# Kernel optimization log

Hardware: AMD Instinct MI355X
Metric: run time of the kernel (lower is better)

The kernel has to match this reference:

```python
import jax, jax.numpy as jnp
import numpy as np

D_MODEL = 512
NUM_HEADS = 8
NUM_LAYERS = 4
SEQ_LEN = 2048
BATCH = 2
LN_EPS = 1e-5


def _layer_norm(x, g, b):
    mu = jnp.mean(x, axis=-1, keepdims=True)
    var = jnp.mean(jnp.square(x - mu), axis=-1, keepdims=True)
    return (x - mu) * jax.lax.rsqrt(var + LN_EPS) * g + b


def setup_inputs() -> dict:
    key = jax.random.key(0)
    ks = jax.random.split(key, 12)
    d, nl = D_MODEL, NUM_LAYERS
    s = 0.02
    return {
        "x": jax.random.normal(ks[0], (BATCH, SEQ_LEN, d), dtype=jnp.float32),
        "mask": jnp.zeros((1, 1, SEQ_LEN, SEQ_LEN), dtype=jnp.float32),
        "Wqkv": jax.random.normal(ks[1], (nl, d, 3 * d), dtype=jnp.float32) * s,
        "Wout": jax.random.normal(ks[2], (nl, d, d), dtype=jnp.float32) * s,
        "ln_g": jnp.ones((nl, d), dtype=jnp.float32),
        "ln_b": jnp.zeros((nl, d), dtype=jnp.float32),
        "W1": jax.random.normal(ks[3], (nl, d, 4 * d), dtype=jnp.float32) * s,
        "b1": jnp.zeros((nl, 4 * d), dtype=jnp.float32),
        "alpha": jnp.full((nl,), 0.01, dtype=jnp.float32),  # PReLU(init=0.01), scalar per block
        "W2": jax.random.normal(ks[4], (nl, 4 * d, d), dtype=jnp.float32) * s,
        "b2": jnp.zeros((nl, d), dtype=jnp.float32),
        "lnf_g": jnp.ones((d,), dtype=jnp.float32),
        "lnf_b": jnp.zeros((d,), dtype=jnp.float32),
    }


def _encoder(x, mask, Wqkv, Wout, ln_g, ln_b, W1, b1, alpha, W2, b2, lnf_g, lnf_b):
    B, L, d = x.shape
    H = NUM_HEADS
    dh = d // H
    scale = 1.0 / (d ** 0.5)  # NOTE: scales by sqrt(d_model), not head dim (as in source)

    def block(x, p):
        wqkv, wout, g, b, w1, b1_, a, w2, b2_ = p
        qkv = x @ wqkv  # [B, L, 3d]
        q, k, v = jnp.split(qkv, 3, axis=-1)
        # b l (h j) -> b h l j
        to_heads = lambda t: t.reshape(B, L, H, dh).transpose(0, 2, 1, 3)
        q, k, v = to_heads(q) * scale, to_heads(k), to_heads(v)
        e = jnp.einsum('bhlj,bhkj->bhlk', q, k) + mask  # [B, H, L, L]
        att = jnp.nan_to_num(jax.nn.softmax(e, axis=-1))
        # Faithful to source: repeated index takes the DIAGONAL of att,
        # then multiplies elementwise into v (NOT a matmul).
        out = jnp.einsum('bhll,bhlj->bhlj', att, v)
        out = out.transpose(0, 2, 1, 3).reshape(B, L, d)  # b h l j -> b l (h j)
        out = out @ wout
        out_att = _layer_norm(out + x, g, b)
        h = out_att @ w1 + b1_
        h = jnp.where(h >= 0, h, a * h)  # PReLU (dropout=0 in eval)
        h = h @ w2 + b2_
        # same LayerNorm params reused (same nn.LayerNorm instance in source)
        return _layer_norm(h + out_att, g, b), None

    params = (Wqkv, Wout, ln_g, ln_b, W1, b1, alpha, W2, b2)
    x, _ = jax.lax.scan(block, x, params)
    return _layer_norm(x, lnf_g, lnf_b)


def reference(x, mask, Wqkv, Wout, ln_g, ln_b, W1, b1, alpha, W2, b2, lnf_g, lnf_b):
    return _encoder(x, mask, Wqkv, Wout, ln_g, ln_b, W1, b1, alpha, W2, b2, lnf_g, lnf_b)
```

## Files before the change

### kernel.cpp

```cpp
#include <hip/hip_runtime.h>
#include <math.h>

typedef unsigned short u16;
typedef __attribute__((ext_vector_type(8))) short short8;
typedef __attribute__((ext_vector_type(4))) float f32x4;

#define SEQ 2048
#define NHEADS 8
#define NLAYERS 4
#define NROWS 4096
#define SCALE_QK 0.044194173824159216f
#define SCALE_QK_LOG2E 0.06376571201f
#define PART_STRIDE ((size_t)NROWS * 512)

#define GLOAD_LDS(gp, lp) __builtin_amdgcn_global_load_lds( \
    (const __attribute__((address_space(1))) uint4*)(gp), \
    (__attribute__((address_space(3))) uint4*)(lp), 16, 0, 0)

__device__ __forceinline__ float b2f(u16 u){
    union { unsigned int i; float f; } c; c.i = ((unsigned int)u) << 16; return c.f;
}
__device__ __forceinline__ u16 f2b(float f){
    union { float f; unsigned int i; } c; c.f = f;
    unsigned int x = c.i;
    unsigned int r = x + 0x7fffu + ((x >> 16) & 1u);
    return (u16)(r >> 16);
}
__device__ __forceinline__ void unpack8(uint4 u, float* f){
    f[0]=b2f(u.x & 0xffffu); f[1]=b2f(u.x >> 16);
    f[2]=b2f(u.y & 0xffffu); f[3]=b2f(u.y >> 16);
    f[4]=b2f(u.z & 0xffffu); f[5]=b2f(u.z >> 16);
    f[6]=b2f(u.w & 0xffffu); f[7]=b2f(u.w >> 16);
}
__device__ __forceinline__ uint4 pack8(const float* f){
    uint4 u;
    u.x = (unsigned)f2b(f[0]) | ((unsigned)f2b(f[1]) << 16);
    u.y = (unsigned)f2b(f[2]) | ((unsigned)f2b(f[3]) << 16);
    u.z = (unsigned)f2b(f[4]) | ((unsigned)f2b(f[5]) << 16);
    u.w = (unsigned)f2b(f[6]) | ((unsigned)f2b(f[7]) << 16);
    return u;
}

__global__ __launch_bounds__(256)
void cvt_f32_bf16(const float* __restrict__ in, u16* __restrict__ out, int n8){
    int i = blockIdx.x * 256 + threadIdx.x;
    if (i >= n8) return;
    const float4* p = (const float4*)(in + (size_t)i * 8);
    float4 a = p[0], b = p[1];
    float f[8] = {a.x, a.y, a.z, a.w, b.x, b.y, b.z, b.w};
    *((uint4*)(out + (size_t)i * 8)) = pack8(f);
}

__global__ __launch_bounds__(256)
void transpose_layer(const float* __restrict__ wqkv, const float* __restrict__ wout,
                     const float* __restrict__ w1,  const float* __restrict__ w2,
                     u16* __restrict__ qkvT, u16* __restrict__ woutT,
                     u16* __restrict__ w1T,  u16* __restrict__ w2T)
{
    __shared__ float tile[32][33];
    int tid = blockIdx.x;
    const float* src; u16* dst; int R, C, local;
    if (tid < 768)       { src = wqkv; dst = qkvT; R = 512;  C = 1536; local = tid; }
    else if (tid < 1024) { src = wout; dst = woutT; R = 512; C = 512;  local = tid - 768; }
    else if (tid < 2048) { src = w1;   dst = w1T;  R = 512;  C = 2048; local = tid - 1024; }
    else                 { src = w2;   dst = w2T;  R = 2048; C = 512;  local = tid - 2048; }
    int ctiles = C >> 5;
    int c0 = (local % ctiles) * 32, r0 = (local / ctiles) * 32;
    int tx = threadIdx.x & 31, ty = threadIdx.x >> 5;
#pragma unroll
    for (int i = 0; i < 4; i++){
        int r = r0 + ty + i * 8;
        tile[ty + i * 8][tx] = src[(size_t)r * C + c0 + tx];
    }
    __syncthreads();
#pragma unroll
    for (int i = 0; i < 4; i++){
        int c = c0 + ty + i * 8;
        dst[(size_t)c * R + r0 + tx] = f2b(tile[tx][ty + i * 8]);
    }
}

template<int BM, int BN, int SPLITS, bool BF16OUT>
__global__ __launch_bounds__(256)
void gemm3(const u16* __restrict__ A, const u16* __restrict__ Bt,
           float* __restrict__ Cf, u16* __restrict__ Cb,
           const float* __restrict__ bias, const float* __restrict__ alphap,
           int M, int N, int K)
{
    constexpr int WAVES_M = BM / 64;
    constexpr int WAVES_N = 4 / WAVES_M;
    constexpr int WN = BN / WAVES_N;
    constexpr int MT = 4, NT = WN / 16;
    __shared__ __align__(16) u16 As[BM * 64];
    __shared__ __align__(16) u16 Bs[BN * 64];

    const int t = threadIdx.x;
    const int wave = t >> 6, lane = t & 63;
    const int quad = lane >> 4, l16 = lane & 15;
    const int wm = (WAVES_M == 2) ? (wave >> 1) : 0;
    const int wn = (WAVES_M == 2) ? (wave & 1) : wave;
    const int n0 = blockIdx.x * BN;
    const int m0 = blockIdx.y * BM;
    const int lr = lane >> 3;
    const int lc = (lane & 7) << 3;
    const int Ks = K / SPLITS;
    const int kbeg = blockIdx.z * Ks;

    f32x4 acc[MT][NT];
#pragma unroll
    for (int i = 0; i < MT; i++)
#pragma unroll
        for (int j = 0; j < NT; j++) acc[i][j] = (f32x4){0.f, 0.f, 0.f, 0.f};

    for (int kt = kbeg; kt < kbeg + Ks; kt += 64){
        __syncthreads();
#pragma unroll
        for (int j = 0; j < BM / 32; j++){
            int r0 = wave * 8 + j * 32;
            GLOAD_LDS(A + (size_t)(m0 + r0 + lr) * K + kt + lc, As + r0 * 64);
        }
#pragma unroll
        for (int j = 0; j < BN / 32; j++){
            int r0 = wave * 8 + j * 32;
            GLOAD_LDS(Bt + (size_t)(n0 + r0 + lr) * K + kt + lc, Bs + r0 * 64);
        }
        __syncthreads();
#pragma unroll
        for (int ks = 0; ks < 2; ks++){
            short8 af[MT], bf[NT];
#pragma unroll
            for (int mt = 0; mt < MT; mt++)
                af[mt] = *((const short8*)&As[(wm * 64 + mt * 16 + l16) * 64 + ks * 32 + quad * 8]);
#pragma unroll
            for (int nt = 0; nt < NT; nt++)
                bf[nt] = *((const short8*)&Bs[(wn * WN + nt * 16 + l16) * 64 + ks * 32 + quad * 8]);
#pragma unroll
            for (int mt = 0; mt < MT; mt++)
#pragma unroll
                for (int nt = 0; nt < NT; nt++)
                    acc[mt][nt] = __builtin_amdgcn_mfma_f32_16x16x32_bf16(af[mt], bf[nt], acc[mt][nt], 0, 0, 0);
        }
    }

    if (BF16OUT){
        const float aval = alphap ? alphap[0] : 0.f;
#pragma unroll
        for (int nt = 0; nt < NT; nt++){
            int col = n0 + wn * WN + nt * 16 + l16;
            float bv = bias ? bias[col] : 0.f;
#pragma unroll
            for (int mt = 0; mt < MT; mt++){
#pragma unroll
                for (int r = 0; r < 4; r++){
                    int row = m0 + wm * 64 + mt * 16 + quad * 4 + r;
                    float v = acc[mt][nt][r] + bv;
                    if (alphap) v = (v >= 0.f) ? v : aval * v;
                    Cb[(size_t)row * N + col] = f2b(v);
                }
            }
        }
    } else {
        float* Cp = Cf + (size_t)blockIdx.z * PART_STRIDE;
#pragma unroll
        for (int nt = 0; nt < NT; nt++){
            int col = n0 + wn * WN + nt * 16 + l16;
#pragma unroll
            for (int mt = 0; mt < MT; mt++){
#pragma unroll
                for (int r = 0; r < 4; r++){
                    int row = m0 + wm * 64 + mt * 16 + quad * 4 + r;
                    Cp[(size_t)row * N + col] = acc[mt][nt][r];
                }
            }
        }
    }
}

__global__ __launch_bounds__(256)
void diag_kernel(const u16* __restrict__ qkv, float* __restrict__ diag_p)
{
    int wid = blockIdx.x * 4 + (threadIdx.x >> 6);
    int lane = threadIdx.x & 63;
    int bh = wid >> 11, l = wid & 2047;
    int b = bh >> 3, h = bh & 7;
    size_t base = (size_t)(b * SEQ + l) * 1536 + h * 64 + lane;
    float q = b2f(qkv[base]);
    float k = b2f(qkv[base + 512]);
    float p = q * k;
#pragma unroll
    for (int off = 32; off; off >>= 1) p += __shfl_xor(p, off, 64);
    if (lane == 0) diag_p[(size_t)bh * SEQ + l] = exp2f(p * SCALE_QK_LOG2E);
}

__global__ __launch_bounds__(256)
void attn_scores2(const u16* __restrict__ qkv, float* __restrict__ rowsum_parts)
{
    __shared__ __align__(16) u16 Qs[128 * 64];
    __shared__ __align__(16) u16 Ks[128 * 64];
    const int t = threadIdx.x, wave = t >> 6, lane = t & 63;
    const int quad = lane >> 4, l16 = lane & 15;
    const int wm = wave >> 1, wn = wave & 1;
    const int ksp = blockIdx.x, ly = blockIdx.y, bh = blockIdx.z;
    const int b = bh >> 3, h = bh & 7;
    const int lr = lane >> 3, lc = (lane & 7) << 3;
    const size_t qbase = (size_t)(b * SEQ + ly * 128) * 1536 + h * 64;

#pragma unroll
    for (int j = 0; j < 4; j++){
        int r0 = wave * 8 + j * 32;
        GLOAD_LDS(qkv + qbase + (size_t)(r0 + lr) * 1536 + lc, Qs + r0 * 64);
    }

    float rs[4][4];
#pragma unroll
    for (int i = 0; i < 4; i++)
#pragma unroll
        for (int j = 0; j < 4; j++) rs[i][j] = 0.f;

    for (int kxi = 0; kxi < 4; kxi++){
        const int kx = ksp * 4 + kxi;
        const size_t kbase = (size_t)(b * SEQ + kx * 128) * 1536 + 512 + h * 64;
        __syncthreads();
#pragma unroll
        for (int j = 0; j < 4; j++){
            int r0 = wave * 8 + j * 32;
            GLOAD_LDS(qkv + kbase + (size_t)(r0 + lr) * 1536 + lc, Ks + r0 * 64);
        }
        __syncthreads();

        f32x4 acc[4][4];
#pragma unroll
        for (int i = 0; i < 4; i++)
#pragma unroll
            for (int j = 0; j < 4; j++) acc[i][j] = (f32x4){0.f, 0.f, 0.f, 0.f};
#pragma unroll
        for (int ks = 0; ks < 2; ks++){
            short8 af[4], bf[4];
#pragma unroll
            for (int mt = 0; mt < 4; mt++)
                af[mt] = *((const short8*)&Qs[(wm * 64 + mt * 16 + l16) * 64 + ks * 32 + quad * 8]);
#pragma unroll
            for (int nt = 0; nt < 4; nt++)
                bf[nt] = *((const short8*)&Ks[(wn * 64 + nt * 16 + l16) * 64 + ks * 32 + quad * 8]);
#pragma unroll
            for (int mt = 0; mt < 4; mt++)
#pragma unroll
                for (int nt = 0; nt < 4; nt++)
                    acc[mt][nt] = __builtin_amdgcn_mfma_f32_16x16x32_bf16(af[mt], bf[nt], acc[mt][nt], 0, 0, 0);
        }
#pragma unroll
        for (int mt = 0; mt < 4; mt++)
#pragma unroll
            for (int nt = 0; nt < 4; nt++)
#pragma unroll
                for (int r = 0; r < 4; r++)
                    rs[mt][r] += exp2f(acc[mt][nt][r] * SCALE_QK_LOG2E);
    }

#pragma unroll
    for (int off = 1; off < 16; off <<= 1){
#pragma unroll
        for (int mt = 0; mt < 4; mt++)
#pragma unroll
            for (int r = 0; r < 4; r++)
                rs[mt][r] += __shfl_xor(rs[mt][r], off, 64);
    }
    if (l16 == 0){
        const int part = ksp * 2 + wn;
        float* dst = rowsum_parts + (size_t)part * 16 * SEQ + (size_t)bh * SEQ + ly * 128;
#pragma unroll
        for (int mt = 0; mt < 4; mt++)
#pragma unroll
            for (int r = 0; r < 4; r++)
                dst[wm * 64 + mt * 16 + quad * 4 + r] = rs[mt][r];
    }
}

__global__ __launch_bounds__(256)
void attn_scale(const u16* __restrict__ qkv, const float* __restrict__ diag_p,
                const float* __restrict__ rowsum_parts, u16* __restrict__ attnb)
{
    int gid = blockIdx.x * 256 + threadIdx.x;
    int row = gid >> 6;
    int col = (gid & 63) << 3;
    int head = col >> 6;
    int b = row >> 11, l = row & 2047;
    size_t idx = (size_t)(b * 8 + head) * SEQ + l;
    float rsum = 0.f;
#pragma unroll
    for (int p = 0; p < 8; p++) rsum += rowsum_parts[(size_t)p * 16 * SEQ + idx];
    float a = diag_p[idx] / rsum;
    uint4 vv = *((const uint4*)(qkv + (size_t)row * 1536 + 1024 + col));
    float f[8]; unpack8(vv, f);
#pragma unroll
    for (int j = 0; j < 8; j++) f[j] *= a;
    *((uint4*)(attnb + (size_t)row * 512 + col)) = pack8(f);
}

__global__ __launch_bounds__(256)
void ln_kernel(const float* __restrict__ res, int nparts,
               const float* __restrict__ bias, const u16* __restrict__ xin,
               const float* __restrict__ gg, const float* __restrict__ bb,
               u16* __restrict__ outb, float* __restrict__ outf)
{
    const int row = blockIdx.x * 4 + (threadIdx.x >> 6);
    const int lane = threadIdx.x & 63;
    const size_t base = (size_t)row * 512 + lane * 8;

    float v[8];
    unpack8(*((const uint4*)(xin + base)), v);
    for (int p = 0; p < nparts; p++){
        const float4* rp = (const float4*)(res + (size_t)p * PART_STRIDE + base);
        float4 r0 = rp[0], r1 = rp[1];
        v[0] += r0.x; v[1] += r0.y; v[2] += r0.z; v[3] += r0.w;
        v[4] += r1.x; v[5] += r1.y; v[6] += r1.z; v[7] += r1.w;
    }
    if (bias){
        const float4* bp4 = (const float4*)(bias + lane * 8);
        float4 c0 = bp4[0], c1 = bp4[1];
        v[0] += c0.x; v[1] += c0.y; v[2] += c0.z; v[3] += c0.w;
        v[4] += c1.x; v[5] += c1.y; v[6] += c1.z; v[7] += c1.w;
    }
    float s = 0.f;
#pragma unroll
    for (int j = 0; j < 8; j++) s += v[j];
#pragma unroll
    for (int off = 32; off; off >>= 1) s += __shfl_xor(s, off, 64);
    float mu = s * (1.f / 512.f);
    float q = 0.f;
#pragma unroll
    for (int j = 0; j < 8; j++){ float d = v[j] - mu; q += d * d; }
#pragma unroll
    for (int off = 32; off; off >>= 1) q += __shfl_xor(q, off, 64);
    float rs = rsqrtf(q * (1.f / 512.f) + 1e-5f);

    const float4* gp = (const float4*)(gg + lane * 8);
    const float4* bp = (const float4*)(bb + lane * 8);
    float4 g0 = gp[0], g1 = gp[1], bb0 = bp[0], bb1 = bp[1];
    float gv[8] = {g0.x, g0.y, g0.z, g0.w, g1.x, g1.y, g1.z, g1.w};
    float bv[8] = {bb0.x, bb0.y, bb0.z, bb0.w, bb1.x, bb1.y, bb1.z, bb1.w};
    float o[8];
#pragma unroll
    for (int j = 0; j < 8; j++) o[j] = (v[j] - mu) * rs * gv[j] + bv[j];
    if (outb){
        *((uint4*)(outb + base)) = pack8(o);
    } else {
        float4* op = (float4*)(outf + base);
        op[0] = make_float4(o[0], o[1], o[2], o[3]);
        op[1] = make_float4(o[4], o[5], o[6], o[7]);
    }
}

extern "C" void kernel_launch(void* const* d_in, const int* in_sizes, int n_in,
                              void* d_out, int out_size, void* d_ws, size_t ws_size,
                              hipStream_t stream)
{
    const float* x_in  = (const float*)d_in[0];
    const float* Wqkv  = (const float*)d_in[2];
    const float* Wout  = (const float*)d_in[3];
    const float* ln_g  = (const float*)d_in[4];
    const float* ln_b  = (const float*)d_in[5];
    const float* W1    = (const float*)d_in[6];
    const float* b1    = (const float*)d_in[7];
    const float* alpha = (const float*)d_in[8];
    const float* W2    = (const float*)d_in[9];
    const float* b2    = (const float*)d_in[10];
    const float* lnf_g = (const float*)d_in[11];
    const float* lnf_b = (const float*)d_in[12];
    float* out = (float*)d_out;

    char* w = (char*)d_ws;
    u16* qkvT  = (u16*)w;  w += (size_t)1536 * 512 * 2;
    u16* woutT = (u16*)w;  w += (size_t)512 * 512 * 2;
    u16* w1T   = (u16*)w;  w += (size_t)2048 * 512 * 2;
    u16* w2T   = (u16*)w;  w += (size_t)512 * 2048 * 2;
    u16* big    = (u16*)w;  w += (size_t)NROWS * 2048 * 2;
    u16* x_cur  = (u16*)w;  w += (size_t)NROWS * 512 * 2;
    u16* attnb  = (u16*)w;  w += (size_t)NROWS * 512 * 2;
    u16* outatt = (u16*)w;  w += (size_t)NROWS * 512 * 2;
    float* tmpf = (float*)w; w += (size_t)4 * PART_STRIDE * 4;
    float* diag_p = (float*)w;       w += (size_t)2 * NHEADS * SEQ * 4;
    float* rowsum_parts = (float*)w; w += (size_t)8 * 2 * NHEADS * SEQ * 4;

    u16* qkvb = big;
    u16* hbuf = big;

    cvt_f32_bf16<<<NROWS * 512 / 8 / 256, 256, 0, stream>>>(x_in, x_cur, NROWS * 512 / 8);

    for (int l = 0; l < NLAYERS; l++){
        transpose_layer<<<3072, 256, 0, stream>>>(
            Wqkv + (size_t)l * 512 * 1536, Wout + (size_t)l * 512 * 512,
            W1 + (size_t)l * 512 * 2048,  W2 + (size_t)l * 2048 * 512,
            qkvT, woutT, w1T, w2T);

        gemm3<128, 64, 1, true><<<dim3(1536 / 64, NROWS / 128), 256, 0, stream>>>(
            x_cur, qkvT, nullptr, qkvb, nullptr, nullptr, NROWS, 1536, 512);

        diag_kernel<<<2 * NHEADS * SEQ / 4, 256, 0, stream>>>(qkvb, diag_p);
        attn_scores2<<<dim3(4, SEQ / 128, 2 * NHEADS), 256, 0, stream>>>(qkvb, rowsum_parts);
        attn_scale<<<NROWS * 512 / 8 / 256, 256, 0, stream>>>(qkvb, diag_p, rowsum_parts, attnb);

        gemm3<64, 128, 2, false><<<dim3(512 / 128, NROWS / 64, 2), 256, 0, stream>>>(
            attnb, woutT, tmpf, nullptr, nullptr, nullptr, NROWS, 512, 512);

        ln_kernel<<<NROWS / 4, 256, 0, stream>>>(tmpf, 2, nullptr, x_cur,
            ln_g + l * 512, ln_b + l * 512, outatt, nullptr);

        gemm3<128, 128, 1, true><<<dim3(2048 / 128, NROWS / 128), 256, 0, stream>>>(
            outatt, w1T, nullptr, hbuf, b1 + (size_t)l * 2048, alpha + l, NROWS, 2048, 512);

        gemm3<64, 128, 4, false><<<dim3(512 / 128, NROWS / 64, 4), 256, 0, stream>>>(
            hbuf, w2T, tmpf, nullptr, nullptr, nullptr, NROWS, 512, 2048);

        ln_kernel<<<NROWS / 4, 256, 0, stream>>>(tmpf, 4, b2 + (size_t)l * 512, outatt,
            ln_g + l * 512, ln_b + l * 512, x_cur, nullptr);
    }

    ln_kernel<<<NROWS / 4, 256, 0, stream>>>(nullptr, 0, nullptr, x_cur, lnf_g, lnf_b, nullptr, out);
}
```

Before: 596.8 us.

## Store split-K partials in bf16, fold diag into attn_scale, reorder block ids

Split-K GEMM partial sums are now written as bf16 instead of fp32, which halves partial-buffer traffic into the layernorm kernels at some cost in accumulated precision. The separate diagonal-score kernel is removed, and attn_scale now computes the q·k dot product directly from the q and k rows it already loads, which saves a launch and an intermediate buffer. GEMM and attention-score grids are flattened to 1D with M-fastest (or bh-fastest) block ordering, so consecutive blocks share the same weight tile for better L2 reuse.

After: 537.5 us. 9.9% less time.

```diff
diff --git a/kernel.cpp b/kernel.cpp
--- a/kernel.cpp
+++ b/kernel.cpp
@@ -9,7 +9,6 @@
 #define NHEADS 8
 #define NLAYERS 4
 #define NROWS 4096
-#define SCALE_QK 0.044194173824159216f
 #define SCALE_QK_LOG2E 0.06376571201f
 #define PART_STRIDE ((size_t)NROWS * 512)
 
@@ -80,13 +79,14 @@
     }
 }
 
-template<int BM, int BN, int SPLITS, bool BF16OUT>
+template<int BM, int BN, int SPLITS>
 __global__ __launch_bounds__(256)
 void gemm3(const u16* __restrict__ A, const u16* __restrict__ Bt,
-           float* __restrict__ Cf, u16* __restrict__ Cb,
+           u16* __restrict__ C,
            const float* __restrict__ bias, const float* __restrict__ alphap,
-           int M, int N, int K)
-{
+           int N, int K)
+{
+    constexpr int NBY = NROWS / BM;
     constexpr int WAVES_M = BM / 64;
     constexpr int WAVES_N = 4 / WAVES_M;
     constexpr int WN = BN / WAVES_N;
@@ -99,8 +99,9 @@
     const int quad = lane >> 4, l16 = lane & 15;
     const int wm = (WAVES_M == 2) ? (wave >> 1) : 0;
     const int wn = (WAVES_M == 2) ? (wave & 1) : wave;
-    const int n0 = blockIdx.x * BN;
-    const int m0 = blockIdx.y * BM;
+    const int id = blockIdx.x;
+    const int m0 = (id % NBY) * BM;
+    const int n0 = (id / NBY) * BN;
     const int lr = lane >> 3;
     const int lc = (lane & 7) << 3;
     const int Ks = K / SPLITS;
@@ -142,54 +143,23 @@
         }
     }
 
-    if (BF16OUT){
-        const float aval = alphap ? alphap[0] : 0.f;
-#pragma unroll
-        for (int nt = 0; nt < NT; nt++){
-            int col = n0 + wn * WN + nt * 16 + l16;
-            float bv = bias ? bias[col] : 0.f;
-#pragma unroll
-            for (int mt = 0; mt < MT; mt++){
-#pragma unroll
-                for (int r = 0; r < 4; r++){
-                    int row = m0 + wm * 64 + mt * 16 + quad * 4 + r;
-                    float v = acc[mt][nt][r] + bv;
-                    if (alphap) v = (v >= 0.f) ? v : aval * v;
-                    Cb[(size_t)row * N + col] = f2b(v);
-                }
+    u16* Cp = (SPLITS > 1) ? (C + (size_t)blockIdx.z * PART_STRIDE) : C;
+    const float aval = alphap ? alphap[0] : 0.f;
+#pragma unroll
+    for (int nt = 0; nt < NT; nt++){
+        int col = n0 + wn * WN + nt * 16 + l16;
+        float bv = (SPLITS == 1 && bias) ? bias[col] : 0.f;
+#pragma unroll
+        for (int mt = 0; mt < MT; mt++){
+#pragma unroll
+            for (int r = 0; r < 4; r++){
+                int row = m0 + wm * 64 + mt * 16 + quad * 4 + r;
+                float v = acc[mt][nt][r] + bv;
+                if (SPLITS == 1 && alphap) v = (v >= 0.f) ? v : aval * v;
+                Cp[(size_t)row * N + col] = f2b(v);
             }
         }
-    } else {
-        float* Cp = Cf + (size_t)blockIdx.z * PART_STRIDE;
-#pragma unroll
-        for (int nt = 0; nt < NT; nt++){
-            int col = n0 + wn * WN + nt * 16 + l16;
-#pragma unroll
-            for (int mt = 0; mt < MT; mt++){
-#pragma unroll
-                for (int r = 0; r < 4; r++){
-                    int row = m0 + wm * 64 + mt * 16 + quad * 4 + r;
-                    Cp[(size_t)row * N + col] = acc[mt][nt][r];
-                }
-            }
-        }
-    }
-}
-
-__global__ __launch_bounds__(256)
-void diag_kernel(const u16* __restrict__ qkv, float* __restrict__ diag_p)
-{
-    int wid = blockIdx.x * 4 + (threadIdx.x >> 6);
-    int lane = threadIdx.x & 63;
-    int bh = wid >> 11, l = wid & 2047;
-    int b = bh >> 3, h = bh & 7;
-    size_t base = (size_t)(b * SEQ + l) * 1536 + h * 64 + lane;
-    float q = b2f(qkv[base]);
-    float k = b2f(qkv[base + 512]);
-    float p = q * k;
-#pragma unroll
-    for (int off = 32; off; off >>= 1) p += __shfl_xor(p, off, 64);
-    if (lane == 0) diag_p[(size_t)bh * SEQ + l] = exp2f(p * SCALE_QK_LOG2E);
+    }
 }
 
 __global__ __launch_bounds__(256)
@@ -200,7 +170,8 @@
     const int t = threadIdx.x, wave = t >> 6, lane = t & 63;
     const int quad = lane >> 4, l16 = lane & 15;
     const int wm = wave >> 1, wn = wave & 1;
-    const int ksp = blockIdx.x, ly = blockIdx.y, bh = blockIdx.z;
+    const int id = blockIdx.x;
+    const int bh = id & 15, ly = (id >> 4) & 15, ksp = id >> 8;
     const int b = bh >> 3, h = bh & 7;
     const int lr = lane >> 3, lc = (lane & 7) << 3;
     const size_t qbase = (size_t)(b * SEQ + ly * 128) * 1536 + h * 64;
@@ -277,28 +248,40 @@
 }
 
 __global__ __launch_bounds__(256)
-void attn_scale(const u16* __restrict__ qkv, const float* __restrict__ diag_p,
-                const float* __restrict__ rowsum_parts, u16* __restrict__ attnb)
+void attn_scale(const u16* __restrict__ qkv, const float* __restrict__ rowsum_parts,
+                u16* __restrict__ attnb)
 {
     int gid = blockIdx.x * 256 + threadIdx.x;
     int row = gid >> 6;
     int col = (gid & 63) << 3;
     int head = col >> 6;
     int b = row >> 11, l = row & 2047;
+    size_t base = (size_t)row * 1536 + col;
+
+    float qv[8], kv[8];
+    unpack8(*((const uint4*)(qkv + base)), qv);
+    unpack8(*((const uint4*)(qkv + base + 512)), kv);
+    float dot = 0.f;
+#pragma unroll
+    for (int j = 0; j < 8; j++) dot += qv[j] * kv[j];
+#pragma unroll
+    for (int off = 1; off < 8; off <<= 1) dot += __shfl_xor(dot, off, 64);
+
     size_t idx = (size_t)(b * 8 + head) * SEQ + l;
     float rsum = 0.f;
 #pragma unroll
     for (int p = 0; p < 8; p++) rsum += rowsum_parts[(size_t)p * 16 * SEQ + idx];
-    float a = diag_p[idx] / rsum;
-    uint4 vv = *((const uint4*)(qkv + (size_t)row * 1536 + 1024 + col));
-    float f[8]; unpack8(vv, f);
+    float a = exp2f(dot * SCALE_QK_LOG2E) / rsum;
+
+    float f[8];
+    unpack8(*((const uint4*)(qkv + base + 1024)), f);
 #pragma unroll
     for (int j = 0; j < 8; j++) f[j] *= a;
     *((uint4*)(attnb + (size_t)row * 512 + col)) = pack8(f);
 }
 
 __global__ __launch_bounds__(256)
-void ln_kernel(const float* __restrict__ res, int nparts,
+void ln_kernel(const u16* __restrict__ res, int nparts,
                const float* __restrict__ bias, const u16* __restrict__ xin,
                const float* __restrict__ gg, const float* __restrict__ bb,
                u16* __restrict__ outb, float* __restrict__ outf)
@@ -310,10 +293,10 @@
     float v[8];
     unpack8(*((const uint4*)(xin + base)), v);
     for (int p = 0; p < nparts; p++){
-        const float4* rp = (const float4*)(res + (size_t)p * PART_STRIDE + base);
-        float4 r0 = rp[0], r1 = rp[1];
-        v[0] += r0.x; v[1] += r0.y; v[2] += r0.z; v[3] += r0.w;
-        v[4] += r1.x; v[5] += r1.y; v[6] += r1.z; v[7] += r1.w;
+        float rv[8];
+        unpack8(*((const uint4*)(res + (size_t)p * PART_STRIDE + base)), rv);
+#pragma unroll
+        for (int j = 0; j < 8; j++) v[j] += rv[j];
     }
     if (bias){
         const float4* bp4 = (const float4*)(bias + lane * 8);
@@ -378,8 +361,7 @@
     u16* x_cur  = (u16*)w;  w += (size_t)NROWS * 512 * 2;
     u16* attnb  = (u16*)w;  w += (size_t)NROWS * 512 * 2;
     u16* outatt = (u16*)w;  w += (size_t)NROWS * 512 * 2;
-    float* tmpf = (float*)w; w += (size_t)4 * PART_STRIDE * 4;
-    float* diag_p = (float*)w;       w += (size_t)2 * NHEADS * SEQ * 4;
+    u16* tmpb   = (u16*)w;  w += (size_t)4 * PART_STRIDE * 2;
     float* rowsum_parts = (float*)w; w += (size_t)8 * 2 * NHEADS * SEQ * 4;
 
     u16* qkvb = big;
@@ -393,26 +375,25 @@
             W1 + (size_t)l * 512 * 2048,  W2 + (size_t)l * 2048 * 512,
             qkvT, woutT, w1T, w2T);
 
-        gemm3<128, 64, 1, true><<<dim3(1536 / 64, NROWS / 128), 256, 0, stream>>>(
-            x_cur, qkvT, nullptr, qkvb, nullptr, nullptr, NROWS, 1536, 512);
-
-        diag_kernel<<<2 * NHEADS * SEQ / 4, 256, 0, stream>>>(qkvb, diag_p);
-        attn_scores2<<<dim3(4, SEQ / 128, 2 * NHEADS), 256, 0, stream>>>(qkvb, rowsum_parts);
-        attn_scale<<<NROWS * 512 / 8 / 256, 256, 0, stream>>>(qkvb, diag_p, rowsum_parts, attnb);
-
-        gemm3<64, 128, 2, false><<<dim3(512 / 128, NROWS / 64, 2), 256, 0, stream>>>(
-            attnb, woutT, tmpf, nullptr, nullptr, nullptr, NROWS, 512, 512);
-
-        ln_kernel<<<NROWS / 4, 256, 0, stream>>>(tmpf, 2, nullptr, x_cur,
+        gemm3<128, 64, 1><<<dim3(24 * 32), 256, 0, stream>>>(
+            x_cur, qkvT, qkvb, nullptr, nullptr, 1536, 512);
+
+        attn_scores2<<<1024, 256, 0, stream>>>(qkvb, rowsum_parts);
+        attn_scale<<<NROWS * 512 / 8 / 256, 256, 0, stream>>>(qkvb, rowsum_parts, attnb);
+
+        gemm3<64, 128, 2><<<dim3(4 * 64, 1, 2), 256, 0, stream>>>(
+            attnb, woutT, tmpb, nullptr, nullptr, 512, 512);
+
+        ln_kernel<<<NROWS / 4, 256, 0, stream>>>(tmpb, 2, nullptr, x_cur,
             ln_g + l * 512, ln_b + l * 512, outatt, nullptr);
 
-        gemm3<128, 128, 1, true><<<dim3(2048 / 128, NROWS / 128), 256, 0, stream>>>(
-            outatt, w1T, nullptr, hbuf, b1 + (size_t)l * 2048, alpha + l, NROWS, 2048, 512);
-
-        gemm3<64, 128, 4, false><<<dim3(512 / 128, NROWS / 64, 4), 256, 0, stream>>>(
-            hbuf, w2T, tmpf, nullptr, nullptr, nullptr, NROWS, 512, 2048);
-
-        ln_kernel<<<NROWS / 4, 256, 0, stream>>>(tmpf, 4, b2 + (size_t)l * 512, outatt,
+        gemm3<128, 128, 1><<<dim3(16 * 32), 256, 0, stream>>>(
+            outatt, w1T, hbuf, b1 + (size_t)l * 2048, alpha + l, 2048, 512);
+
+        gemm3<64, 128, 4><<<dim3(4 * 64, 1, 4), 256, 0, stream>>>(
+            hbuf, w2T, tmpb, nullptr, nullptr, 512, 2048);
+
+        ln_kernel<<<NROWS / 4, 256, 0, stream>>>(tmpb, 4, b2 + (size_t)l * 512, outatt,
             ln_g + l * 512, ln_b + l * 512, x_cur, nullptr);
     }
 
```
